# Optimization experiments

Hardware: AMD Instinct MI355X
Metric: run time of the kernel (lower is better)

The kernel has to match this reference:

```python
import jax, jax.numpy as jnp
import numpy as np

GAMMA = 1.0e6  # sigmoid sharpness for soft histogram


def _dct_basis():
    # Standard orthonormal 8x8 2D DCT-II basis, laid out as [64, 1, 8, 8] (OIHW).
    i = np.arange(8)
    a = np.where(i == 0, np.sqrt(1.0 / 8.0), np.sqrt(2.0 / 8.0))
    cos = np.cos((2 * i[None, :] + 1) * i[:, None] * np.pi / 16.0)  # [freq, pos]
    basis = np.einsum('u,v,ui,vj->uvij', a, a, cos, cos).reshape(64, 1, 8, 8)
    return jnp.asarray(basis, jnp.float32)


def _conv(x, w, stride=1, pad=0):
    return jax.lax.conv_general_dilated(
        x, w, (stride, stride), [(pad, pad), (pad, pad)],
        dimension_numbers=('NCHW', 'OIHW', 'NCHW'))


def _bn(x, g, b, eps=1e-5):
    # BatchNorm2d in training mode: batch statistics over (N, H, W).
    m = x.mean((0, 2, 3), keepdims=True)
    v = x.var((0, 2, 3), keepdims=True)
    return g[None, :, None, None] * (x - m) * jax.lax.rsqrt(v + eps) + b[None, :, None, None]


def _pool2(x):
    return jax.lax.reduce_window(x, -jnp.inf, jax.lax.max,
                                 (1, 1, 2, 2), (1, 1, 2, 2), 'VALID')


def setup_inputs() -> dict:
    key = jax.random.key(0)
    ks = jax.random.split(key, 16)
    B = 64

    def n(k, shape, scale=0.05):
        return jax.random.normal(k, shape, jnp.float32) * scale

    FC1_IN = 15 * 8 * 256 + 64  # 30784
    return {
        'x': jax.random.normal(ks[0], (B, 1, 256, 256), jnp.float32),
        'qvectors': jax.random.uniform(ks[1], (B, 64), dtype=jnp.float32),
        'dct_basis': _dct_basis(),
        'w1a': n(ks[2], (64, 1, 5, 5)), 'b1a': jnp.zeros(64, jnp.float32),
        'g1a': jnp.ones(64, jnp.float32), 'be1a': jnp.zeros(64, jnp.float32),
        'w1b': n(ks[3], (64, 64, 5, 5)), 'b1b': jnp.zeros(64, jnp.float32),
        'g1b': jnp.ones(64, jnp.float32), 'be1b': jnp.zeros(64, jnp.float32),
        'w2a': n(ks[4], (128, 64, 5, 5)), 'b2a': jnp.zeros(128, jnp.float32),
        'g2a': jnp.ones(128, jnp.float32), 'be2a': jnp.zeros(128, jnp.float32),
        'w3a': n(ks[5], (256, 128, 5, 5)), 'b3a': jnp.zeros(256, jnp.float32),
        'g3a': jnp.ones(256, jnp.float32), 'be3a': jnp.zeros(256, jnp.float32),
        'fc1_w': n(ks[6], (500, FC1_IN), 0.02), 'fc1_b': jnp.zeros(500, jnp.float32),
        'fc2_w': n(ks[7], (500, 564), 0.02), 'fc2_b': jnp.zeros(500, jnp.float32),
        'fc3_w': n(ks[8], (2, 564), 0.02), 'fc3_b': jnp.zeros(2, jnp.float32),
    }


def reference(x, qvectors, dct_basis,
              w1a, b1a, g1a, be1a,
              w1b, b1b, g1b, be1b,
              w2a, b2a, g2a, be2a,
              w3a, b3a, g3a, be3a,
              fc1_w, fc1_b, fc2_w, fc2_b, fc3_w, fc3_b):
    # --- no_grad block: DCT + 121-bin soft histogram ---
    xd = _conv(x, dct_basis, stride=8)  # [B, 64, 32, 32]
    bins = jnp.arange(-60, 61, dtype=xd.dtype)  # 121 thresholds

    def step(_, b):
        h = jnp.sum(jax.nn.sigmoid(GAMMA * (xd - b)), axis=(2, 3)) / 1024.0  # [B, 64]
        return None, h

    _, hist = jax.lax.scan(step, None, bins)        # [121, B, 64]
    hist = jnp.transpose(hist, (1, 0, 2))           # [B, 121, 64]
    feat = hist[:, 0:120, :] - hist[:, 1:121, :]    # per-bin soft counts
    feat = jax.lax.stop_gradient(feat.reshape(-1, 1, 120, 64))

    # --- CNN stack ---
    h = jax.nn.relu(_bn(_conv(feat, w1a, pad=2) + b1a[None, :, None, None], g1a, be1a))
    h = jax.nn.relu(_bn(_conv(h, w1b, pad=2) + b1b[None, :, None, None], g1b, be1b))
    h = _pool2(h)  # [B, 64, 60, 32]
    h = jax.nn.relu(_bn(_conv(h, w2a, pad=2) + b2a[None, :, None, None], g2a, be2a))
    h = _pool2(h)  # [B, 128, 30, 16]
    h = jax.nn.relu(_bn(_conv(h, w3a, pad=2) + b3a[None, :, None, None], g3a, be3a))
    h = _pool2(h)  # [B, 256, 15, 8]

    # --- MLP head with qvector concats ---
    hf = h.reshape(-1, 15 * 8 * 256)
    z = jax.nn.relu(jnp.concatenate([qvectors, hf], axis=1) @ fc1_w.T + fc1_b)
    z = jax.nn.relu(jnp.concatenate([qvectors, z], axis=1) @ fc2_w.T + fc2_b)
    return jnp.concatenate([qvectors, z], axis=1) @ fc3_w.T + fc3_b  # [B, 2]
```

## Files before the change

kernel.cpp:

```cpp
#include <hip/hip_runtime.h>
#include <math.h>


typedef __attribute__((ext_vector_type(8))) _Float16 f16x8;
typedef __attribute__((ext_vector_type(4))) float f32x4;

#define GAMMA_F 1.0e6f

__device__ __forceinline__ unsigned short f2h(float f) {
  _Float16 h = (_Float16)f;
  union { _Float16 h; unsigned short u; } x; x.h = h; return x.u;
}
__device__ __forceinline__ float h2f(unsigned short u) {
  union { unsigned short u; _Float16 h; } x; x.u = u; return (float)x.h;
}

__global__ __launch_bounds__(256) void k_dct(const float* __restrict__ x,
                                             const float* __restrict__ basis,
                                             float* __restrict__ xd) {
  __shared__ float bT[4096];
  __shared__ float pix[4][64];
  int tid = threadIdx.x;
  for (int e = tid; e < 4096; e += 256)
    bT[e] = basis[(e & 63) * 64 + (e >> 6)];
  __syncthreads();
  int w = tid >> 6, lane = tid & 63;
  int b = blockIdx.x >> 3;
  int br = ((blockIdx.x & 7) << 2) + w;
  const float* xb = x + (size_t)b * 65536;
  float* xdb = xd + (size_t)b * 65536;
  for (int bc = 0; bc < 32; ++bc) {
    __syncthreads();
    pix[w][lane] = xb[(br * 8 + (lane >> 3)) * 256 + bc * 8 + (lane & 7)];
    __syncthreads();
    float acc = 0.f;
#pragma unroll
    for (int p = 0; p < 64; ++p)
      acc = fmaf(bT[p * 64 + lane], pix[w][p], acc);
    xdb[lane * 1024 + br * 32 + bc] = acc;
  }
}

__global__ __launch_bounds__(256) void k_hist(const float* __restrict__ xd,
                                              float* __restrict__ feat) {
  __shared__ float px[1024];
  __shared__ float part[242];
  __shared__ float tot[121];
  int tid = threadIdx.x;
  int bc = blockIdx.x;
  int b = bc >> 6, c = bc & 63;
  const float* p = xd + (size_t)bc * 1024;
  for (int e = tid; e < 1024; e += 256) px[e] = p[e];
  __syncthreads();
  if (tid < 242) {
    int j = tid >> 1;
    float bj = (float)(j - 60);
    int i0 = (tid & 1) * 512;
    float cnt = 0.f;
    for (int i = i0; i < i0 + 512; ++i) {
      float d = px[i] - bj;
      float step = d > 0.f ? 1.f : 0.f;
      cnt += step;
      if (fabsf(d) < 2e-5f)
        cnt += 1.f / (1.f + expf(-GAMMA_F * d)) - step;
    }
    part[tid] = cnt;
  }
  __syncthreads();
  if (tid < 121) tot[tid] = part[2 * tid] + part[2 * tid + 1];
  __syncthreads();
  if (tid < 120)
    feat[((size_t)b * 120 + tid) * 64 + c] = (tot[tid] - tot[tid + 1]) * (1.f / 1024.f);
}

__global__ __launch_bounds__(256) void k_prepw(const float* __restrict__ w,
                                               unsigned short* __restrict__ wt,
                                               int OC, int IC) {
  int n = OC * IC * 25;
  int idx = blockIdx.x * 256 + threadIdx.x;
  if (idx >= n) return;
  int j = idx & 7;
  int q = (idx >> 3) & 3;
  int l15 = (idx >> 5) & 15;
  int r = idx >> 9;
  int icb = r % (IC / 32);
  int r2 = r / (IC / 32);
  int mt = r2 % (OC / 16);
  int t = r2 / (OC / 16);
  int oc = mt * 16 + l15;
  int ic = icb * 32 + q * 8 + j;
  wt[idx] = f2h(w[((size_t)oc * IC + ic) * 25 + t]);
}

__global__ __launch_bounds__(256) void k_conv1a(const float* __restrict__ in,
                                                const float* __restrict__ wgt,
                                                unsigned short* __restrict__ out) {
  __shared__ float tile[20 * 21];
  int tx = threadIdx.x & 15, ty = threadIdx.x >> 4;
  int tileX = (blockIdx.x & 3) * 16, tileY = (blockIdx.x >> 2) * 16;
  int b = blockIdx.y, ocb = blockIdx.z * 8;
  const float* inc = in + (size_t)b * 7680;
  for (int e = threadIdx.x; e < 400; e += 256) {
    int ly = e / 20, lx = e % 20;
    int gy = tileY - 2 + ly, gx = tileX - 2 + lx;
    float v = 0.f;
    if ((unsigned)gy < 120u && (unsigned)gx < 64u) v = inc[gy * 64 + gx];
    tile[ly * 21 + lx] = v;
  }
  __syncthreads();
  float tv[25];
#pragma unroll
  for (int dy = 0; dy < 5; ++dy)
#pragma unroll
    for (int dx = 0; dx < 5; ++dx)
      tv[dy * 5 + dx] = tile[(ty + dy) * 21 + tx + dx];
  float acc[8];
#pragma unroll
  for (int o = 0; o < 8; ++o) {
    const float* wo = wgt + (size_t)(ocb + o) * 25;
    float a = 0.f;
#pragma unroll
    for (int t = 0; t < 25; ++t) a = fmaf(tv[t], wo[t], a);
    acc[o] = a;
  }
  int oy = tileY + ty, ox = tileX + tx;
  if (oy < 120) {
    size_t base = (((size_t)b * 120 + oy) * 64 + ox) * 64 + ocb;
    ushort4 p0, p1;
    p0.x = f2h(acc[0]); p0.y = f2h(acc[1]); p0.z = f2h(acc[2]); p0.w = f2h(acc[3]);
    p1.x = f2h(acc[4]); p1.y = f2h(acc[5]); p1.z = f2h(acc[6]); p1.w = f2h(acc[7]);
    *(ushort4*)(out + base) = p0;
    *(ushort4*)(out + base + 4) = p1;
  }
}

template <int CIN, int H, int W, int TC, int NT, int OC, bool PREBN>
__global__ __launch_bounds__(256, 4) void k_convM(const unsigned short* __restrict__ in,
                                                  const unsigned short* __restrict__ wt,
                                                  unsigned short* __restrict__ out,
                                                  const float* __restrict__ pst,
                                                  const float* __restrict__ pg,
                                                  const float* __restrict__ pbe) {
  constexpr int XC = TC / 16, RPW = NT / XC, WGR = 4 * RPW;
  constexpr int LW = TC + 4, LR = WGR + 4, NPX = LR * LW;
  constexpr int NXC = W / TC;
  constexpr int MTS = (CIN / 32) * 512;
  constexpr int TS = (OC / 16) * MTS;
  __shared__ unsigned short lds[NPX * 40];
  int tid = threadIdx.x;
  int w = tid >> 6, lane = tid & 63, l15 = lane & 15, q = lane >> 4;
  int q4 = tid & 3;
  int ry = blockIdx.x / NXC, cx = blockIdx.x % NXC;
  int y0 = ry * WGR, x0 = cx * TC;
  int b = blockIdx.y, oc0 = blockIdx.z * 64;
  int z4 = blockIdx.z * 4;
  int lofs = (l15 * 4 + q) * 8;
  f32x4 acc[4][NT];
#pragma unroll
  for (int mt = 0; mt < 4; ++mt)
#pragma unroll
    for (int nt = 0; nt < NT; ++nt) acc[mt][nt] = 0.f;

  for (int icb = 0; icb < CIN / 32; ++icb) {
    float s8[8], a8[8];
    if (PREBN) {
      int cb = icb * 32 + q4 * 8;
#pragma unroll
      for (int j = 0; j < 8; ++j) {
        float m = pst[cb + j], iv = pst[CIN + cb + j];
        s8[j] = pg[cb + j] * iv;
        a8[j] = pbe[cb + j] - m * s8[j];
      }
    }
    __syncthreads();
    for (int e = tid; e < NPX * 4; e += 256) {
      int px = e >> 2;
      int lr = px / LW, c = px % LW;
      int y = y0 - 2 + lr, x = x0 - 2 + c;
      f16x8 v = (f16x8)0;
      if ((unsigned)y < (unsigned)H && (unsigned)x < (unsigned)W) {
        v = *(const f16x8*)(in + (((size_t)b * H + y) * W + x) * CIN + icb * 32 + q4 * 8);
        if (PREBN) {
#pragma unroll
          for (int j = 0; j < 8; ++j) {
            float f = fmaf((float)v[j], s8[j], a8[j]);
            v[j] = (_Float16)(f > 0.f ? f : 0.f);
          }
        }
      }
      *(f16x8*)&lds[(size_t)(px * 5 + q4) * 8] = v;
    }
    __syncthreads();
    const unsigned short* wbase = wt + (size_t)icb * 512 + lofs;
    f16x8 avn[4];
#pragma unroll
    for (int mt = 0; mt < 4; ++mt)
      avn[mt] = *(const f16x8*)(wbase + (size_t)(z4 + mt) * MTS);
#pragma unroll
    for (int t = 0; t < 25; ++t) {
      int dy = t / 5, dx = t % 5;
      f16x8 avc[4];
#pragma unroll
      for (int mt = 0; mt < 4; ++mt) avc[mt] = avn[mt];
      if (t < 24) {
#pragma unroll
        for (int mt = 0; mt < 4; ++mt)
          avn[mt] = *(const f16x8*)(wbase + (size_t)(t + 1) * TS + (size_t)(z4 + mt) * MTS);
      }
#pragma unroll
      for (int nt = 0; nt < NT; ++nt) {
        int lr = w * RPW + nt / XC + dy;
        int c = (nt % XC) * 16 + l15 + dx;
        f16x8 bv = *(const f16x8*)&lds[(size_t)((lr * LW + c) * 5 + q) * 8];
#pragma unroll
        for (int mt = 0; mt < 4; ++mt)
          acc[mt][nt] = __builtin_amdgcn_mfma_f32_16x16x32_f16(avc[mt], bv, acc[mt][nt], 0, 0, 0);
      }
    }
  }
#pragma unroll
  for (int nt = 0; nt < NT; ++nt) {
    int y = y0 + w * RPW + nt / XC;
    if (y >= H) continue;
    int x = x0 + (nt % XC) * 16 + l15;
    size_t pbase = (((size_t)b * H + y) * W + x) * OC + oc0 + q * 4;
#pragma unroll
    for (int mt = 0; mt < 4; ++mt) {
      ushort4 pk;
      pk.x = f2h(acc[mt][nt][0]);
      pk.y = f2h(acc[mt][nt][1]);
      pk.z = f2h(acc[mt][nt][2]);
      pk.w = f2h(acc[mt][nt][3]);
      *(ushort4*)(out + pbase + mt * 16) = pk;
    }
  }
}

template <int C>
__global__ __launch_bounds__(256) void k_bnstatsv(const unsigned short* __restrict__ x,
                                                  float* __restrict__ acc,
                                                  int nIter) {
  constexpr int CV = C / 8, KPB = 256 / CV;
  __shared__ float r1[256][8], r2[256][8];
  int tid = threadIdx.x;
  int cv = tid % CV, kq = tid / CV;
  size_t row0 = (size_t)blockIdx.x * (KPB * nIter) + kq;
  const unsigned short* p = x + row0 * C + cv * 8;
  float s1[8], s2[8];
#pragma unroll
  for (int j = 0; j < 8; ++j) { s1[j] = 0.f; s2[j] = 0.f; }
  for (int it = 0; it < nIter; ++it) {
    f16x8 v = *(const f16x8*)(p + (size_t)it * KPB * C);
#pragma unroll
    for (int j = 0; j < 8; ++j) {
      float f = (float)v[j];
      s1[j] += f;
      s2[j] += f * f;
    }
  }
#pragma unroll
  for (int j = 0; j < 8; ++j) { r1[tid][j] = s1[j]; r2[tid][j] = s2[j]; }
  __syncthreads();
  if (tid < C) {
    int cv0 = tid >> 3, e = tid & 7;
    float t1 = 0.f, t2 = 0.f;
    for (int k = 0; k < KPB; ++k) {
      t1 += r1[k * CV + cv0][e];
      t2 += r2[k * CV + cv0][e];
    }
    atomicAdd(&acc[tid], t1);
    atomicAdd(&acc[C + tid], t2);
  }
}

__global__ __launch_bounds__(256) void k_bnfin(const float* __restrict__ acc,
                                               float* __restrict__ stats,
                                               int C, float invN) {
  int c = threadIdx.x + blockIdx.x * 256;
  if (c >= C) return;
  float m = acc[c] * invN;
  float v = acc[C + c] * invN - m * m;
  stats[c] = m;
  stats[C + c] = rsqrtf(v + 1e-5f);
}

template <int C, int H, int W>
__global__ __launch_bounds__(256) void k_brp(const unsigned short* __restrict__ x,
                                             unsigned short* __restrict__ y,
                                             const float* __restrict__ stats,
                                             const float* __restrict__ g,
                                             const float* __restrict__ be) {
  constexpr int OH = H / 2, OW = W / 2, CV = C / 8;
  int idx = blockIdx.x * 256 + threadIdx.x;
  int cv = idx % CV;
  int t = idx / CV;
  int ox = t % OW; t /= OW;
  int oy = t % OH;
  int b = t / OH;
  int c0 = cv * 8;
  const unsigned short* p = x + ((size_t)(b * H + oy * 2) * W + ox * 2) * C + c0;
  f16x8 v00 = *(const f16x8*)p;
  f16x8 v01 = *(const f16x8*)(p + C);
  f16x8 v10 = *(const f16x8*)(p + (size_t)W * C);
  f16x8 v11 = *(const f16x8*)(p + (size_t)W * C + C);
  f16x8 r;
#pragma unroll
  for (int j = 0; j < 8; ++j) {
    int c = c0 + j;
    float m = stats[c], iv = stats[C + c], gg = g[c], bb = be[c];
    float f0 = gg * (((float)v00[j] - m) * iv) + bb;
    float f1 = gg * (((float)v01[j] - m) * iv) + bb;
    float f2 = gg * (((float)v10[j] - m) * iv) + bb;
    float f3 = gg * (((float)v11[j] - m) * iv) + bb;
    f0 = f0 > 0.f ? f0 : 0.f;
    f1 = f1 > 0.f ? f1 : 0.f;
    f2 = f2 > 0.f ? f2 : 0.f;
    f3 = f3 > 0.f ? f3 : 0.f;
    float r01 = f0 > f1 ? f0 : f1;
    float r23 = f2 > f3 ? f2 : f3;
    r[j] = (_Float16)(r01 > r23 ? r01 : r23);
  }
  *(f16x8*)(y + (size_t)idx * 8) = r;
}

__global__ __launch_bounds__(256) void k_brp3t(const unsigned short* __restrict__ x,
                                               unsigned short* __restrict__ actT,
                                               const float* __restrict__ stats,
                                               const float* __restrict__ g,
                                               const float* __restrict__ be) {
  __shared__ float tile[64 * 65];
  int s = blockIdx.x;
  int oy = s >> 3, ox = s & 7;
  int ci = threadIdx.x & 63, bq = threadIdx.x >> 6;
  for (int cs = 0; cs < 4; ++cs) {
    int c = cs * 64 + ci;
    float m = stats[c], iv = stats[256 + c], gg = g[c], bb = be[c];
    __syncthreads();
    for (int b = bq; b < 64; b += 4) {
      float mx = 0.f;
#pragma unroll
      for (int qq = 0; qq < 4; ++qq) {
        int yy = oy * 2 + (qq >> 1), xx = ox * 2 + (qq & 1);
        float v = h2f(x[((size_t)(b * 30 + yy) * 16 + xx) * 256 + c]);
        v = gg * ((v - m) * iv) + bb;
        v = v > 0.f ? v : 0.f;
        mx = v > mx ? v : mx;
      }
      tile[ci * 65 + b] = mx;
    }
    __syncthreads();
    for (int e = threadIdx.x; e < 4096; e += 256) {
      int cc = e >> 6, bb2 = e & 63;
      actT[(size_t)bb2 * 30784 + 64 + (cs * 64 + cc) * 120 + s] = f2h(tile[cc * 65 + bb2]);
    }
  }
}

__global__ __launch_bounds__(256) void k_qinit(const float* __restrict__ q,
                                               unsigned short* __restrict__ actT,
                                               float* __restrict__ in2T,
                                               float* __restrict__ in3T,
                                               float* __restrict__ z1pre,
                                               float* __restrict__ bnacc) {
  int idx = blockIdx.x * 256 + threadIdx.x;
  if (idx < 32000) z1pre[idx] = 0.f;
  else if (idx < 33024) bnacc[idx - 32000] = 0.f;
  if (idx >= 4096) return;
  int b = idx >> 6, i = idx & 63;
  float v = q[idx];
  actT[(size_t)b * 30784 + i] = f2h(v);
  in2T[i * 64 + b] = v;
  in3T[i * 64 + b] = v;
}

__global__ __launch_bounds__(256) void k_fc1m(const unsigned short* __restrict__ actT,
                                              const float* __restrict__ wgt,
                                              float* __restrict__ z1pre) {
  constexpr int IN = 30784;
  constexpr int KSTEPS = IN / 32;
  __shared__ float part[4][16][64];
  int tid = threadIdx.x;
  int w = tid >> 6, lane = tid & 63, l15 = lane & 15, q = lane >> 4;
  int ob = blockIdx.x * 16;
  int row = ob + l15; if (row > 499) row = 499;
  int kw = blockIdx.y * 4 + w;
  f32x4 acc[4];
#pragma unroll
  for (int nt = 0; nt < 4; ++nt) acc[nt] = 0.f;
  for (int s = kw; s < KSTEPS; s += 32) {
    int k0 = s * 32;
    const float4* wp = (const float4*)(wgt + (size_t)row * IN + k0 + q * 8);
    float4 wa = wp[0], wb = wp[1];
    f16x8 a;
    a[0] = (_Float16)wa.x; a[1] = (_Float16)wa.y;
    a[2] = (_Float16)wa.z; a[3] = (_Float16)wa.w;
    a[4] = (_Float16)wb.x; a[5] = (_Float16)wb.y;
    a[6] = (_Float16)wb.z; a[7] = (_Float16)wb.w;
#pragma unroll
    for (int nt = 0; nt < 4; ++nt) {
      f16x8 bv = *(const f16x8*)(actT + (size_t)(nt * 16 + l15) * IN + k0 + q * 8);
      acc[nt] = __builtin_amdgcn_mfma_f32_16x16x32_f16(a, bv, acc[nt], 0, 0, 0);
    }
  }
#pragma unroll
  for (int nt = 0; nt < 4; ++nt)
#pragma unroll
    for (int reg = 0; reg < 4; ++reg)
      part[w][q * 4 + reg][nt * 16 + l15] = acc[nt][reg];
  __syncthreads();
  for (int e = tid; e < 1024; e += 256) {
    int m = e >> 6, n = e & 63;
    float sum = part[0][m][n] + part[1][m][n] + part[2][m][n] + part[3][m][n];
    int o = ob + m;
    if (o < 500) atomicAdd(&z1pre[o * 64 + n], sum);
  }
}

__global__ __launch_bounds__(256) void k_fc1ep(const float* __restrict__ z1pre,
                                               const float* __restrict__ bias,
                                               float* __restrict__ in2T) {
  int idx = blockIdx.x * 256 + threadIdx.x;
  if (idx >= 500 * 64) return;
  int o = idx >> 6;
  float v = z1pre[idx] + bias[o];
  in2T[idx + 64 * 64] = v > 0.f ? v : 0.f;
}

__global__ __launch_bounds__(256) void k_fc_small(const float* __restrict__ inT,
                                                  const float* __restrict__ wgt,
                                                  const float* __restrict__ bias,
                                                  float* __restrict__ out,
                                                  int IN, int mode) {
  __shared__ float part[4][64];
  int o = blockIdx.x;
  int lane = threadIdx.x & 63, w = threadIdx.x >> 6;
  float acc = 0.f;
  for (int i = w; i < IN; i += 4)
    acc = fmaf(inT[(size_t)i * 64 + lane], wgt[(size_t)o * IN + i], acc);
  part[w][lane] = acc;
  __syncthreads();
  if (threadIdx.x < 64) {
    float s = part[0][lane] + part[1][lane] + part[2][lane] + part[3][lane] + bias[o];
    if (mode == 0) {
      s = s > 0.f ? s : 0.f;
      out[(64 + o) * 64 + lane] = s;
    } else {
      out[lane * 2 + o] = s;
    }
  }
}

extern "C" void kernel_launch(void* const* d_in, const int* in_sizes, int n_in,
                              void* d_out, int out_size, void* d_ws, size_t ws_size,
                              hipStream_t stream) {
  const float* x      = (const float*)d_in[0];
  const float* qvec   = (const float*)d_in[1];
  const float* basis  = (const float*)d_in[2];
  const float* w1a    = (const float*)d_in[3];
  const float* g1a    = (const float*)d_in[5];
  const float* be1a   = (const float*)d_in[6];
  const float* w1b    = (const float*)d_in[7];
  const float* g1b    = (const float*)d_in[9];
  const float* be1b   = (const float*)d_in[10];
  const float* w2a    = (const float*)d_in[11];
  const float* g2a    = (const float*)d_in[13];
  const float* be2a   = (const float*)d_in[14];
  const float* w3a    = (const float*)d_in[15];
  const float* g3a    = (const float*)d_in[17];
  const float* be3a   = (const float*)d_in[18];
  const float* fc1w   = (const float*)d_in[19];
  const float* fc1b   = (const float*)d_in[20];
  const float* fc2w   = (const float*)d_in[21];
  const float* fc2b   = (const float*)d_in[22];
  const float* fc3w   = (const float*)d_in[23];
  const float* fc3b   = (const float*)d_in[24];
  float* out = (float*)d_out;

  char* base = (char*)d_ws;
  constexpr size_t ARENA = 62914560;
  char* arenaA = base;
  char* arenaB = base + ARENA;
  char* sm     = base + 2 * ARENA;

  float*          xd   = (float*)arenaA;
  unsigned short* A    = (unsigned short*)arenaA;
  unsigned short* P1   = (unsigned short*)arenaA;
  unsigned short* P2   = (unsigned short*)arenaA;
  unsigned short* actT = (unsigned short*)arenaA;

  float*          feat = (float*)arenaB;
  unsigned short* Bb   = (unsigned short*)arenaB;
  unsigned short* C2   = (unsigned short*)arenaB;
  unsigned short* D3   = (unsigned short*)arenaB;

  float* in2T = (float*)sm;
  float* in3T = (float*)(sm + 144384);
  float* z1p  = (float*)(sm + 288768);
  float* ACC  = (float*)(sm + 416768);
  float* S1A  = (float*)(sm + 420864);
  float* S1B  = (float*)(sm + 421376);
  float* S2A  = (float*)(sm + 421888);
  float* S3A  = (float*)(sm + 422912);
  unsigned short* WT1 = (unsigned short*)(sm + 424960);
  unsigned short* WT2 = (unsigned short*)(sm + 834560);
  unsigned short* WT3 = (unsigned short*)(sm + 1653760);

  k_qinit<<<130, 256, 0, stream>>>(qvec, actT, in2T, in3T, z1p, ACC);
  k_prepw<<<400, 256, 0, stream>>>(w1b, WT1, 64, 64);
  k_prepw<<<800, 256, 0, stream>>>(w2a, WT2, 128, 64);
  k_prepw<<<3200, 256, 0, stream>>>(w3a, WT3, 256, 128);

  k_dct<<<64 * 8, 256, 0, stream>>>(x, basis, xd);
  k_hist<<<4096, 256, 0, stream>>>(xd, feat);

  k_conv1a<<<dim3(32, 64, 8), 256, 0, stream>>>(feat, w1a, A);
  k_bnstatsv<64><<<240, 256, 0, stream>>>(A, ACC, 64);
  k_bnfin<<<1, 64, 0, stream>>>(ACC, S1A, 64, 1.f / 491520.f);

  k_convM<64, 120, 64, 32, 4, 64, true><<<dim3(30, 64, 1), 256, 0, stream>>>(
      A, WT1, Bb, S1A, g1a, be1a);
  k_bnstatsv<64><<<240, 256, 0, stream>>>(Bb, ACC + 128, 64);
  k_bnfin<<<1, 64, 0, stream>>>(ACC + 128, S1B, 64, 1.f / 491520.f);
  k_brp<64, 120, 64><<<3840, 256, 0, stream>>>(Bb, P1, S1B, g1b, be1b);

  k_convM<64, 60, 32, 32, 4, 128, false><<<dim3(8, 64, 2), 256, 0, stream>>>(
      P1, WT2, C2, S1A, g1a, be1a);
  k_bnstatsv<128><<<240, 256, 0, stream>>>(C2, ACC + 256, 32);
  k_bnfin<<<1, 128, 0, stream>>>(ACC + 256, S2A, 128, 1.f / 122880.f);
  k_brp<128, 60, 32><<<1920, 256, 0, stream>>>(C2, P2, S2A, g2a, be2a);

  k_convM<128, 30, 16, 16, 2, 256, false><<<dim3(4, 64, 4), 256, 0, stream>>>(
      P2, WT3, D3, S1A, g1a, be1a);
  k_bnstatsv<256><<<240, 256, 0, stream>>>(D3, ACC + 512, 16);
  k_bnfin<<<1, 256, 0, stream>>>(ACC + 512, S3A, 256, 1.f / 30720.f);
  k_qinit<<<130, 256, 0, stream>>>(qvec, actT, in2T, in3T, z1p, ACC);
  k_brp3t<<<120, 256, 0, stream>>>(D3, actT, S3A, g3a, be3a);

  k_fc1m<<<dim3(32, 8), 256, 0, stream>>>(actT, fc1w, z1p);
  k_fc1ep<<<125, 256, 0, stream>>>(z1p, fc1b, in2T);
  k_fc_small<<<500, 256, 0, stream>>>(in2T, fc2w, fc2b, in3T, 564, 0);
  k_fc_small<<<2, 256, 0, stream>>>(in3T, fc3w, fc3b, out, 564, 1);
}
```

Measured before the change: 1.002 ms.

## Replace per-bin sigmoid sweep with direct bin assignment and LDS atomics

The soft-histogram kernel previously made every thread sweep all 1024 values for one of 121 bin edges, giving about 124k compare operations per (batch, channel). It now reads each value once, finds its bin directly with rint/ceil, and applies the sigmoid split only when the value sits within 2e-5 of an integer edge. Counts are accumulated through shared-memory atomics, which adds contention when many values fall in the same bin. The conv kernel's launch_bounds occupancy hint is also lowered from 4 to 3 waves, giving the compiler more registers per thread.

```diff
diff --git a/kernel.cpp b/kernel.cpp
--- a/kernel.cpp
+++ b/kernel.cpp
@@ -43,34 +43,32 @@
 
 __global__ __launch_bounds__(256) void k_hist(const float* __restrict__ xd,
                                               float* __restrict__ feat) {
-  __shared__ float px[1024];
-  __shared__ float part[242];
-  __shared__ float tot[121];
+  __shared__ float h[120];
   int tid = threadIdx.x;
   int bc = blockIdx.x;
   int b = bc >> 6, c = bc & 63;
-  const float* p = xd + (size_t)bc * 1024;
-  for (int e = tid; e < 1024; e += 256) px[e] = p[e];
-  __syncthreads();
-  if (tid < 242) {
-    int j = tid >> 1;
-    float bj = (float)(j - 60);
-    int i0 = (tid & 1) * 512;
-    float cnt = 0.f;
-    for (int i = i0; i < i0 + 512; ++i) {
-      float d = px[i] - bj;
-      float step = d > 0.f ? 1.f : 0.f;
-      cnt += step;
-      if (fabsf(d) < 2e-5f)
-        cnt += 1.f / (1.f + expf(-GAMMA_F * d)) - step;
-    }
-    part[tid] = cnt;
-  }
-  __syncthreads();
-  if (tid < 121) tot[tid] = part[2 * tid] + part[2 * tid + 1];
+  if (tid < 120) h[tid] = 0.f;
+  __syncthreads();
+  const float4* p4 = (const float4*)(xd + (size_t)bc * 1024);
+  float4 v4 = p4[tid];
+#pragma unroll
+  for (int k = 0; k < 4; ++k) {
+    float pv = k == 0 ? v4.x : (k == 1 ? v4.y : (k == 2 ? v4.z : v4.w));
+    float v = rintf(pv);
+    float d = pv - v;
+    if (fabsf(d) < 2e-5f && v >= -60.f && v <= 60.f) {
+      float s = 1.f / (1.f + expf(-GAMMA_F * d));
+      int vi = (int)v;
+      if (vi >= -59) atomicAdd(&h[vi + 59], 1.f - s);
+      if (vi <= 59)  atomicAdd(&h[vi + 60], s);
+    } else {
+      int j = (int)ceilf(pv + 60.f) - 1;
+      if (j >= 0 && j <= 119) atomicAdd(&h[j], 1.f);
+    }
+  }
   __syncthreads();
   if (tid < 120)
-    feat[((size_t)b * 120 + tid) * 64 + c] = (tot[tid] - tot[tid + 1]) * (1.f / 1024.f);
+    feat[((size_t)b * 120 + tid) * 64 + c] = h[tid] * (1.f / 1024.f);
 }
 
 __global__ __launch_bounds__(256) void k_prepw(const float* __restrict__ w,
@@ -135,7 +133,7 @@
 }
 
 template <int CIN, int H, int W, int TC, int NT, int OC, bool PREBN>
-__global__ __launch_bounds__(256, 4) void k_convM(const unsigned short* __restrict__ in,
+__global__ __launch_bounds__(256, 3) void k_convM(const unsigned short* __restrict__ in,
                                                   const unsigned short* __restrict__ wt,
                                                   unsigned short* __restrict__ out,
                                                   const float* __restrict__ pst,
```

Result: faster. 922.8 us (-7.9%).
